# Kernel tuning notes

Hardware: AMD Instinct MI355X
Metric: run time of the kernel (lower is better)

## Reference

```python
import jax, jax.numpy as jnp
import numpy as np
from math import factorial, sqrt, pi

LMAX, NSH = 2, 9
F = 64
N_RBF = 20
N_INTER = 2
N_ATOMS = 1000
N_PAIRS = 10000
CUTOFF = 5.0

# ---------- Clebsch-Gordan coefficients for real spherical harmonics ----------

def _cg_complex(l1, m1, l2, m2, l3, m3):
    # <l1 m1 l2 m2 | l3 m3> via Racah formula
    if m3 != m1 + m2 or not (abs(l1 - l2) <= l3 <= l1 + l2):
        return 0.0
    f = factorial
    pre = sqrt((2 * l3 + 1) * f(l3 + l1 - l2) * f(l3 - l1 + l2) * f(l1 + l2 - l3) / f(l1 + l2 + l3 + 1))
    pre *= sqrt(f(l3 + m3) * f(l3 - m3) * f(l1 - m1) * f(l1 + m1) * f(l2 - m2) * f(l2 + m2))
    s = 0.0
    for k in range(l1 + l2 - l3 + 1):
        d = [k, l1 + l2 - l3 - k, l1 - m1 - k, l2 + m2 - k, l3 - l2 + m1 + k, l3 - l1 - m2 + k]
        if min(d) < 0:
            continue
        s += (-1) ** k / np.prod([float(f(t)) for t in d])
    return pre * s

def _sh_indices(lmax):
    l = np.concatenate([np.full(2 * ll + 1, ll) for ll in range(lmax + 1)])
    m = np.concatenate([np.arange(-ll, ll + 1) for ll in range(lmax + 1)])
    return l, m

def _real_cg(lmax):
    lidx, midx = _sh_indices(lmax)
    n = (lmax + 1) ** 2
    cgc = np.zeros((n, n, n))
    for a in range(n):
        for b in range(n):
            for c in range(n):
                cgc[a, b, c] = _cg_complex(lidx[a], midx[a], lidx[b], midx[b], lidx[c], midx[c])
    # complex -> real spherical harmonic change of basis (per degree l)
    U = np.zeros((n, n), dtype=np.complex128)
    for ll in range(lmax + 1):
        base = ll * ll + ll
        U[base, base] = 1.0
        for m in range(1, ll + 1):
            U[base + m, base - m] = 1 / sqrt(2)
            U[base + m, base + m] = (-1) ** m / sqrt(2)
            U[base - m, base - m] = 1j / sqrt(2)
            U[base - m, base + m] = -1j * (-1) ** m / sqrt(2)
    cgr = np.einsum('ijk,ai,bj,ck->abc', cgc.astype(np.complex128), U, U, U.conj())
    parity = (-1.0) ** lidx
    mask = (parity[:, None, None] * parity[None, :, None]) == parity[None, None, :]
    cgr = np.real(cgr) * mask
    cgr = np.transpose(cgr, (2, 0, 1))  # [s_out, s_in(x), s_filter(Y)]
    s1, s2, s3 = np.nonzero(np.abs(cgr) > 1e-9)
    return s1, s2, s3, cgr[s1, s2, s3].astype(np.float32), lidx

_S1, _S2, _S3, _CGV, _LIDX = _real_cg(LMAX)
IDX1 = jnp.asarray(_S1)            # output sh channel per CG path
IDX2 = jnp.asarray(_S2)            # input-feature sh channel per CG path
IDX3 = jnp.asarray(_S3)            # Ylm sh channel per CG path
CGVAL = jnp.asarray(_CGV)          # CG value per path
WIDX = jnp.asarray(_LIDX[_S3])     # radial-filter degree per CG path
LIDX = jnp.asarray(_LIDX)          # degree of each of the 9 sh channels

# ---------- real spherical harmonics (lmax=2, orthonormal, m=-l..l order) ----------

def _rsh(u):
    x, y, z = u[:, 0], u[:, 1], u[:, 2]
    c1 = sqrt(3.0 / (4.0 * pi))
    c2 = 0.5 * sqrt(15.0 / pi)
    return jnp.stack([
        jnp.full_like(x, 0.5 / sqrt(pi)),
        c1 * y, c1 * z, c1 * x,
        c2 * x * y,
        c2 * y * z,
        0.25 * sqrt(5.0 / pi) * (3.0 * z * z - 1.0),
        c2 * x * z,
        0.25 * sqrt(15.0 / pi) * (x * x - y * y),
    ], axis=1)


def setup_inputs() -> dict:
    key = jax.random.key(0)
    ks = jax.random.split(key, 10)
    atomic_numbers = jax.random.randint(ks[0], (N_ATOMS,), 0, 100)
    r_ij = 1.5 * jax.random.normal(ks[1], (N_PAIRS, 3), dtype=jnp.float32)
    idx_i = jnp.sort(jax.random.randint(ks[2], (N_PAIRS,), 0, N_ATOMS))
    idx_j = jax.random.randint(ks[3], (N_PAIRS,), 0, N_ATOMS)
    emb = jax.random.normal(ks[4], (100, F), dtype=jnp.float32)
    def s(k, sh, fan):
        return jax.random.normal(k, sh, dtype=jnp.float32) / float(np.sqrt(fan))
    Wf = s(ks[5], (N_INTER, N_RBF, (LMAX + 1) * F), N_RBF)
    bf = jnp.zeros((N_INTER, (LMAX + 1) * F), jnp.float32)
    W1 = s(ks[6], (N_INTER, F, F), F)
    W2 = s(ks[7], (N_INTER, F, F), F)
    W3 = s(ks[8], (N_INTER, F, F), F)
    Wg = s(ks[9], (N_INTER, F, (LMAX + 1) * F), F)
    bg = jnp.zeros((N_INTER, (LMAX + 1) * F), jnp.float32)
    return dict(atomic_numbers=atomic_numbers, r_ij=r_ij, idx_i=idx_i, idx_j=idx_j,
                emb=emb, Wf=Wf, bf=bf, W1=W1, W2=W2, W3=W3, Wg=Wg, bg=bg)


def reference(atomic_numbers, r_ij, idx_i, idx_j, emb, Wf, bf, W1, W2, W3, Wg, bg):
    n_atoms = atomic_numbers.shape[0]
    d = jnp.linalg.norm(r_ij, axis=1, keepdims=True)          # [P,1]
    Yij = _rsh(r_ij / d)                                       # [P,9]
    offsets = jnp.linspace(0.0, CUTOFF, N_RBF)                 # GaussianRBF
    width = CUTOFF / (N_RBF - 1)
    radial = jnp.exp((-0.5 / (width * width)) * (d - offsets) ** 2)   # [P,n_rbf]
    cut = 0.5 * (jnp.cos(d * (pi / CUTOFF)) + 1.0) * (d < CUTOFF)     # [P,1]
    # nuclear embedding + scalar2rsh (zero-pad l>0 channels)
    x = jnp.zeros((n_atoms, NSH, F), emb.dtype).at[:, 0, :].set(emb[atomic_numbers])
    for t in range(N_INTER):
        # SO3Convolution
        Wij = (radial @ Wf[t] + bf[t]).reshape(-1, LMAX + 1, F) * cut[:, :, None]  # [P,lmax+1,F]
        xj = x[idx_j]                                                              # [P,9,F]
        v = xj[:, IDX2] * Yij[:, IDX3, None] * Wij[:, WIDX] * CGVAL[None, :, None]  # [P,nnz,F]
        yij = jnp.zeros_like(xj).at[:, IDX1].add(v)                                 # CG scatter
        dx = jax.ops.segment_sum(yij, idx_i, num_segments=n_atoms)                  # edge->node scatter
        # mixing1 + SO3TensorProduct
        ddx = dx @ W1[t]
        tp = jnp.zeros_like(dx).at[:, IDX1].add(dx[:, IDX2] * ddx[:, IDX3] * CGVAL[None, :, None])
        dx = (dx + tp) @ W2[t]
        # SO3ParametricGatedNonlinearity (gate from l=0 channel)
        gate = (dx[:, 0] @ Wg[t] + bg[t]).reshape(-1, LMAX + 1, F)
        dx = dx * jax.nn.sigmoid(gate[:, LIDX])
        dx = dx @ W3[t]
        x = x + dx
    return x  # multipole_representation [n_atoms, 9, F]; x[:,0] is scalar_representation
```

## Files before the change

### kernel.cpp

```cpp
#include <hip/hip_runtime.h>
#include <cmath>

constexpr int kNsh    = 9;
constexpr int kF      = 64;
constexpr int kNrbf   = 20;
constexpr int kNAtoms = 1000;
constexpr int kNPairs = 10000;
constexpr float kCutoffF = 5.0f;
constexpr int kMaxNZ  = 200;
constexpr int kCp     = 12;
constexpr int kXs     = kF * kCp;
constexpr int kWT     = 68;

struct CGSparse {
  int n;
  int c[kMaxNZ];
  int a[kMaxNZ];
  int b[kMaxNZ];
  float v[kMaxNZ];
};

constexpr double cfact(int n) {
  double r = 1.0;
  for (int i = 2; i <= n; i++) r *= (double)i;
  return r;
}
constexpr double cabs_(double x) { return x < 0 ? -x : x; }
constexpr double csqrt_(double x) {
  if (x <= 0.0) return 0.0;
  double g = x < 1.0 ? 1.0 : x;
  for (int i = 0; i < 60; i++) g = 0.5 * (g + x / g);
  return g;
}

constexpr double cg_cplx(int l1, int m1, int l2, int m2, int l3, int m3) {
  if (m3 != m1 + m2) return 0.0;
  int lo = l1 > l2 ? l1 - l2 : l2 - l1;
  if (l3 < lo || l3 > l1 + l2) return 0.0;
  double pre = csqrt_((2 * l3 + 1) * cfact(l3 + l1 - l2) * cfact(l3 - l1 + l2) *
                      cfact(l1 + l2 - l3) / cfact(l1 + l2 + l3 + 1));
  pre *= csqrt_(cfact(l3 + m3) * cfact(l3 - m3) * cfact(l1 - m1) *
                cfact(l1 + m1) * cfact(l2 - m2) * cfact(l2 + m2));
  double s = 0.0;
  for (int k = 0; k <= l1 + l2 - l3; k++) {
    int d0 = k, d1 = l1 + l2 - l3 - k, d2 = l1 - m1 - k;
    int d3 = l2 + m2 - k, d4 = l3 - l2 + m1 + k, d5 = l3 - l1 - m2 + k;
    if (d0 < 0 || d1 < 0 || d2 < 0 || d3 < 0 || d4 < 0 || d5 < 0) continue;
    double den = cfact(d0) * cfact(d1) * cfact(d2) * cfact(d3) * cfact(d4) * cfact(d5);
    s += ((k % 2) ? -1.0 : 1.0) / den;
  }
  return pre * s;
}

constexpr CGSparse build_cg() {
  CGSparse out{};
  int lidx[9] = {0, 1, 1, 1, 2, 2, 2, 2, 2};
  int midx[9] = {0, -1, 0, 1, -2, -1, 0, 1, 2};
  double Ur[9][9] = {};
  double Ui[9][9] = {};
  for (int l = 0; l <= 2; l++) {
    int base = l * l + l;
    Ur[base][base] = 1.0;
    for (int m = 1; m <= l; m++) {
      double s2 = 1.0 / csqrt_(2.0);
      double sgn = (m % 2) ? -1.0 : 1.0;
      Ur[base + m][base - m] = s2;
      Ur[base + m][base + m] = sgn * s2;
      Ui[base - m][base - m] = s2;
      Ui[base - m][base + m] = -sgn * s2;
    }
  }
  double cgr[9][9][9] = {};
  for (int i = 0; i < 9; i++)
    for (int j = 0; j < 9; j++)
      for (int k = 0; k < 9; k++) {
        double cv = cg_cplx(lidx[i], midx[i], lidx[j], midx[j], lidx[k], midx[k]);
        if (cv == 0.0) continue;
        for (int a2 = 0; a2 < 9; a2++) {
          if (Ur[a2][i] == 0.0 && Ui[a2][i] == 0.0) continue;
          for (int b2 = 0; b2 < 9; b2++) {
            if (Ur[b2][j] == 0.0 && Ui[b2][j] == 0.0) continue;
            for (int c2 = 0; c2 < 9; c2++) {
              if (Ur[c2][k] == 0.0 && Ui[c2][k] == 0.0) continue;
              double ar = Ur[a2][i], ai = Ui[a2][i];
              double br = Ur[b2][j], bi = Ui[b2][j];
              double cr = Ur[c2][k], ci = -Ui[c2][k];
              double pr = ar * br - ai * bi;
              double pi = ar * bi + ai * br;
              double rr = pr * cr - pi * ci;
              cgr[c2][a2][b2] += rr * cv;
            }
          }
        }
      }
  int n = 0;
  for (int c2 = 0; c2 < 9; c2++)
    for (int a2 = 0; a2 < 9; a2++)
      for (int b2 = 0; b2 < 9; b2++) {
        bool mask = ((lidx[a2] + lidx[b2]) % 2) == (lidx[c2] % 2);
        double v = mask ? cgr[c2][a2][b2] : 0.0;
        if (cabs_(v) > 1e-9) {
          out.c[n] = c2;
          out.a[n] = a2;
          out.b[n] = b2;
          out.v[n] = (float)v;
          n++;
        }
      }
  out.n = n;
  return out;
}

constexpr CGSparse CG = build_cg();
static_assert(CG.n > 0 && CG.n <= kMaxNZ, "CG table size out of range");

constexpr int kPreBlkPairs = kNPairs / 8;
constexpr int kPreBlkSeg   = (kNAtoms + 1 + 255) / 256;
constexpr int kPreBlkTotal = kPreBlkPairs + kPreBlkSeg;

__global__ __launch_bounds__(256) void k_pre(
    const float* __restrict__ rij, const int* __restrict__ idx_i,
    float* __restrict__ pd_all, int* __restrict__ seg) {
  const int blk = blockIdx.x;
  if (blk < kPreBlkPairs) {
    int sub = threadIdx.x >> 5;
    int f = threadIdx.x & 31;
    int p = blk * 8 + sub;
    float rx = rij[3 * p + 0], ry = rij[3 * p + 1], rz = rij[3 * p + 2];
    float d = sqrtf(rx * rx + ry * ry + rz * rz);
    float inv = 1.0f / d;
    float x = rx * inv, y = ry * inv, z = rz * inv;
    const float c0 = 0.28209479177387814f;
    const float c1 = 0.4886025119029199f;
    const float c2 = 1.0925484305920792f;
    const float c3 = 0.31539156525252005f;
    const float c4 = 0.5462742152960396f;
    float cut = (d < kCutoffF) ? 0.5f * (cosf(d * (float)(M_PI / 5.0)) + 1.0f) : 0.0f;
    float val = 0.f;
    if (f < 9) {
      val =
          (f == 0) ? c0 :
          (f == 1) ? c1 * y :
          (f == 2) ? c1 * z :
          (f == 3) ? c1 * x :
          (f == 4) ? c2 * x * y :
          (f == 5) ? c2 * y * z :
          (f == 6) ? c3 * (3.0f * z * z - 1.0f) :
          (f == 7) ? c2 * x * z :
                     c4 * (x * x - y * y);
    } else if (f == 9) {
      val = cut;
    } else if (f < 30) {
      const float width = kCutoffF / (kNrbf - 1);
      const float coef = -0.5f / (width * width);
      float off = (kCutoffF * (f - 10)) / (kNrbf - 1);
      float tt = d - off;
      val = expf(coef * tt * tt) * cut;
    }
    if (f < 30) pd_all[p * 32 + f] = val;
  } else {
    int a = (blk - kPreBlkPairs) * 256 + threadIdx.x;
    if (a <= kNAtoms) {
      int lo = 0, hi = kNPairs;
      while (lo < hi) {
        int mid = (lo + hi) >> 1;
        if (idx_i[mid] < a) lo = mid + 1; else hi = mid;
      }
      seg[a] = lo;
    }
  }
}

__device__ __forceinline__ void mm_phase(const float* __restrict__ sIn,
                                         const float* __restrict__ W,
                                         float* __restrict__ sRw,
                                         int k0, int cgi, int fb) {
  if (cgi >= 3) return;
  const int c0 = cgi * 4;
  float acc[4][4];
  #pragma unroll
  for (int i = 0; i < 4; i++)
    #pragma unroll
    for (int j = 0; j < 4; j++) acc[i][j] = 0.f;
  #pragma unroll
  for (int half = 0; half < 2; half++) {
    float4 wr[8];
    #pragma unroll
    for (int kk = 0; kk < 8; kk++) {
      wr[kk] = *(const float4*)(W + (k0 + half * 8 + kk) * kF + fb);
    }
    #pragma unroll
    for (int kk = 0; kk < 8; kk++) {
      int k = k0 + half * 8 + kk;
      float4 av = *(const float4*)(sIn + k * kCp + c0);
      float4 wv = wr[kk];
      float a[4] = {av.x, av.y, av.z, av.w};
      float w[4] = {wv.x, wv.y, wv.z, wv.w};
      #pragma unroll
      for (int i = 0; i < 4; i++)
        #pragma unroll
        for (int j = 0; j < 4; j++) acc[i][j] += a[i] * w[j];
    }
  }
  #pragma unroll
  for (int j = 0; j < 4; j++) {
    float4 v = {acc[0][j], acc[1][j], acc[2][j], acc[3][j]};
    *(float4*)(sRw + (fb + j) * kCp + c0) = v;
  }
}

template <int T>
__global__ __launch_bounds__(256) void k_inter(
    const float* __restrict__ pd_all, const float* __restrict__ Wft,
    const float* __restrict__ bft, const int* __restrict__ seg,
    const int* __restrict__ idx_j, const int* __restrict__ Z,
    const float* __restrict__ emb, const float* __restrict__ x_in,
    const float* __restrict__ W1, const float* __restrict__ W2,
    const float* __restrict__ W3, const float* __restrict__ Wg,
    const float* __restrict__ bg, float* __restrict__ x_out) {
  const int atom = blockIdx.x;
  const int tid = threadIdx.x;
  const int wv = tid >> 6;
  const int lane = tid & 63;
  const int cgi = lane >> 4;
  const int fb = (lane & 15) * 4;
  const int k0 = wv * 16;

  __shared__ __align__(16) float sWfT[kF * kWT];
  __shared__ __align__(16) float sA[kF * kCp];
  __shared__ __align__(16) float sR[4][kF * kCp];
  __shared__ __align__(16) float sGp[4][192];

  {
    const float4* g4 = (const float4*)Wft;
    #pragma unroll
    for (int rr = 0; rr < 4; rr++) {
      int i = rr * 256 + tid;
      if (i < kNrbf * 192 / 4) {
        float4 v = g4[i];
        int m = 4 * i;
        int k = m / 192, rem = m % 192;
        int l = rem / 64, f0 = rem % 64;
        int li = l * 20 + k;
        float va[4] = {v.x, v.y, v.z, v.w};
        #pragma unroll
        for (int q = 0; q < 4; q++) sWfT[(f0 + q) * kWT + li] = va[q];
      }
    }
  }
  const float bf0 = bft[lane], bf1 = bft[64 + lane], bf2 = bft[128 + lane];
  __syncthreads();

  {
    float y[12];
    #pragma unroll
    for (int c = 0; c < 12; c++) y[c] = 0.f;
    const int s0 = seg[atom], s1 = seg[atom + 1];
    const float* wrow = sWfT + lane * kWT;
    for (int p0 = s0 + wv; p0 < s1; p0 += 4) {
      const int p = __builtin_amdgcn_readfirstlane(p0);
      const int j = __builtin_amdgcn_readfirstlane(idx_j[p]);
      const float* pd = pd_all + p * 32;
      const float cut = pd[9];
      float Wl[3] = {bf0 * cut, bf1 * cut, bf2 * cut};
      #pragma unroll
      for (int j4 = 0; j4 < 15; j4++) {
        float4 w = *(const float4*)(wrow + 4 * j4);
        float wa[4] = {w.x, w.y, w.z, w.w};
        #pragma unroll
        for (int q = 0; q < 4; q++) {
          constexpr int dummy = 0; (void)dummy;
          int i = 4 * j4 + q;
          Wl[i / 20] += pd[10 + (i % 20)] * wa[q];
        }
      }
      float YW[9];
      YW[0] = pd[0] * Wl[0];
      YW[1] = pd[1] * Wl[1];
      YW[2] = pd[2] * Wl[1];
      YW[3] = pd[3] * Wl[1];
      #pragma unroll
      for (int b = 4; b < 9; b++) YW[b] = pd[b] * Wl[2];
      if (T == 0) {
        float e = emb[Z[j] * kF + lane];
        #pragma unroll
        for (int q = 0; q < CG.n; q++) {
          if (CG.a[q] == 0) y[CG.c[q]] += CG.v[q] * YW[CG.b[q]] * e;
        }
      } else {
        const float* xj = x_in + j * kXs + lane * kCp;
        float xv[12];
        *(float4*)&xv[0] = *(const float4*)(xj + 0);
        *(float4*)&xv[4] = *(const float4*)(xj + 4);
        *(float4*)&xv[8] = *(const float4*)(xj + 8);
        #pragma unroll
        for (int q = 0; q < CG.n; q++) {
          y[CG.c[q]] += CG.v[q] * YW[CG.b[q]] * xv[CG.a[q]];
        }
      }
    }
    float4* r4 = (float4*)(sR[wv] + lane * kCp);
    r4[0] = *(float4*)&y[0];
    r4[1] = *(float4*)&y[4];
    r4[2] = *(float4*)&y[8];
  }
  __syncthreads();
  if (tid < 192) {
    const float4* r0 = (const float4*)sR[0];
    const float4* r1 = (const float4*)sR[1];
    const float4* r2 = (const float4*)sR[2];
    const float4* r3 = (const float4*)sR[3];
    float4 a = r0[tid], b = r1[tid], c = r2[tid], d = r3[tid];
    float4 s = {a.x + b.x + c.x + d.x, a.y + b.y + c.y + d.y,
                a.z + b.z + c.z + d.z, a.w + b.w + c.w + d.w};
    ((float4*)sA)[tid] = s;
  }
  __syncthreads();

  mm_phase(sA, W1, sR[wv], k0, cgi, fb);
  __syncthreads();

  if (wv == 0) {
    float dxv[12], ddx[12];
    {
      const float4* sa = (const float4*)(sA + lane * kCp);
      *(float4*)&dxv[0] = sa[0];
      *(float4*)&dxv[4] = sa[1];
      *(float4*)&dxv[8] = sa[2];
    }
    #pragma unroll
    for (int c = 0; c < 12; c++) {
      ddx[c] = sR[0][lane * kCp + c] + sR[1][lane * kCp + c] +
               sR[2][lane * kCp + c] + sR[3][lane * kCp + c];
    }
    float t2[12];
    #pragma unroll
    for (int c = 0; c < 9; c++) t2[c] = dxv[c];
    t2[9] = 0.f; t2[10] = 0.f; t2[11] = 0.f;
    #pragma unroll
    for (int q = 0; q < CG.n; q++) {
      t2[CG.c[q]] += CG.v[q] * dxv[CG.a[q]] * ddx[CG.b[q]];
    }
    float4* sa = (float4*)(sA + lane * kCp);
    sa[0] = *(float4*)&t2[0];
    sa[1] = *(float4*)&t2[4];
    sa[2] = *(float4*)&t2[8];
  }
  __syncthreads();

  mm_phase(sA, W2, sR[wv], k0, cgi, fb);
  __syncthreads();

  {
    float g0 = 0.f, g1 = 0.f, g2 = 0.f;
    #pragma unroll 4
    for (int kk = 0; kk < 16; kk++) {
      int k = k0 + kk;
      float a = sR[0][k * kCp] + sR[1][k * kCp] + sR[2][k * kCp] + sR[3][k * kCp];
      g0 += a * Wg[k * 192 + lane];
      g1 += a * Wg[k * 192 + 64 + lane];
      g2 += a * Wg[k * 192 + 128 + lane];
    }
    sGp[wv][lane] = g0;
    sGp[wv][64 + lane] = g1;
    sGp[wv][128 + lane] = g2;
  }
  __syncthreads();

  if (wv == 0) {
    float dx2v[12];
    #pragma unroll
    for (int c = 0; c < 12; c++) {
      dx2v[c] = sR[0][lane * kCp + c] + sR[1][lane * kCp + c] +
                sR[2][lane * kCp + c] + sR[3][lane * kCp + c];
    }
    float g0 = bg[lane] + sGp[0][lane] + sGp[1][lane] + sGp[2][lane] + sGp[3][lane];
    float g1 = bg[64 + lane] + sGp[0][64 + lane] + sGp[1][64 + lane] +
               sGp[2][64 + lane] + sGp[3][64 + lane];
    float g2 = bg[128 + lane] + sGp[0][128 + lane] + sGp[1][128 + lane] +
               sGp[2][128 + lane] + sGp[3][128 + lane];
    g0 = 1.f / (1.f + expf(-g0));
    g1 = 1.f / (1.f + expf(-g1));
    g2 = 1.f / (1.f + expf(-g2));
    float dx3[12];
    dx3[0] = dx2v[0] * g0;
    dx3[1] = dx2v[1] * g1;
    dx3[2] = dx2v[2] * g1;
    dx3[3] = dx2v[3] * g1;
    #pragma unroll
    for (int c = 4; c < 9; c++) dx3[c] = dx2v[c] * g2;
    dx3[9] = 0.f; dx3[10] = 0.f; dx3[11] = 0.f;
    float4* sa = (float4*)(sA + lane * kCp);
    sa[0] = *(float4*)&dx3[0];
    sa[1] = *(float4*)&dx3[4];
    sa[2] = *(float4*)&dx3[8];
  }
  __syncthreads();

  mm_phase(sA, W3, sR[wv], k0, cgi, fb);
  __syncthreads();

  if (T == 0) {
    if (tid < 192) {
      const int f = tid / 3, r = tid % 3;
      const float4* r0 = (const float4*)sR[0];
      const float4* r1 = (const float4*)sR[1];
      const float4* r2 = (const float4*)sR[2];
      const float4* r3 = (const float4*)sR[3];
      float4 a = r0[tid], b = r1[tid], c = r2[tid], d = r3[tid];
      float4 s = {a.x + b.x + c.x + d.x, a.y + b.y + c.y + d.y,
                  a.z + b.z + c.z + d.z, a.w + b.w + c.w + d.w};
      if (r == 0) s.x += emb[Z[atom] * kF + f];
      *(float4*)(x_out + atom * kXs + tid * 4) = s;
    }
  } else {
    if (tid < 192) {
      const float4* r0 = (const float4*)sR[0];
      const float4* r1 = (const float4*)sR[1];
      const float4* r2 = (const float4*)sR[2];
      const float4* r3 = (const float4*)sR[3];
      float4 a = r0[tid], b = r1[tid], c = r2[tid], d = r3[tid];
      float4 xi = *(const float4*)(x_in + atom * kXs + tid * 4);
      float4 s = {a.x + b.x + c.x + d.x + xi.x, a.y + b.y + c.y + d.y + xi.y,
                  a.z + b.z + c.z + d.z + xi.z, a.w + b.w + c.w + d.w + xi.w};
      ((float4*)sA)[tid] = s;
    }
    __syncthreads();
    #pragma unroll
    for (int r = 0; r < 3; r++) {
      int i = r * 256 + tid;
      if (i < kNsh * kF) {
        int c = i >> 6, f = i & 63;
        x_out[atom * (kNsh * kF) + i] = sA[f * kCp + c];
      }
    }
  }
}

extern "C" void kernel_launch(void* const* d_in, const int* in_sizes, int n_in,
                              void* d_out, int out_size, void* d_ws, size_t ws_size,
                              hipStream_t stream) {
  const int* Z        = (const int*)d_in[0];
  const float* rij    = (const float*)d_in[1];
  const int* idx_i    = (const int*)d_in[2];
  const int* idx_j    = (const int*)d_in[3];
  const float* emb    = (const float*)d_in[4];
  const float* Wf     = (const float*)d_in[5];
  const float* bf     = (const float*)d_in[6];
  const float* W1     = (const float*)d_in[7];
  const float* W2     = (const float*)d_in[8];
  const float* W3     = (const float*)d_in[9];
  const float* Wg     = (const float*)d_in[10];
  const float* bg     = (const float*)d_in[11];
  float* out = (float*)d_out;

  float* x1  = (float*)d_ws;
  float* pd  = x1 + kNAtoms * kXs;
  int*   seg = (int*)(pd + kNPairs * 32);

  k_pre<<<kPreBlkTotal, 256, 0, stream>>>(rij, idx_i, pd, seg);

  k_inter<0><<<kNAtoms, 256, 0, stream>>>(
      pd, Wf, bf, seg, idx_j, Z, emb, x1,
      W1, W2, W3, Wg, bg, x1);

  k_inter<1><<<kNAtoms, 256, 0, stream>>>(
      pd, Wf + kNrbf * 192, bf + 192, seg, idx_j, Z, emb, x1,
      W1 + kF * kF, W2 + kF * kF, W3 + kF * kF,
      Wg + kF * 192, bg + 192, out);
}
```

Measured before the change: 127.6 us.

## Fuse pair preprocessing and segment search into first interaction kernel

Removes the separate k_pre launch. The first interaction kernel now finds its own atom's segment bounds by binary search and computes the spherical harmonics, cutoff and RBF features for that atom's pairs. It writes them to global memory for the second kernel to reuse, then reads them back in the interaction loop. This saves one kernel launch and its inter-kernel gap. In exchange, each block serializes preprocessing work before its interaction phase and does two redundant binary searches per block boundary.

```diff
diff --git a/kernel.cpp b/kernel.cpp
--- a/kernel.cpp
+++ b/kernel.cpp
@@ -114,59 +114,21 @@
 constexpr CGSparse CG = build_cg();
 static_assert(CG.n > 0 && CG.n <= kMaxNZ, "CG table size out of range");
 
-constexpr int kPreBlkPairs = kNPairs / 8;
-constexpr int kPreBlkSeg   = (kNAtoms + 1 + 255) / 256;
-constexpr int kPreBlkTotal = kPreBlkPairs + kPreBlkSeg;
-
-__global__ __launch_bounds__(256) void k_pre(
-    const float* __restrict__ rij, const int* __restrict__ idx_i,
-    float* __restrict__ pd_all, int* __restrict__ seg) {
-  const int blk = blockIdx.x;
-  if (blk < kPreBlkPairs) {
-    int sub = threadIdx.x >> 5;
-    int f = threadIdx.x & 31;
-    int p = blk * 8 + sub;
-    float rx = rij[3 * p + 0], ry = rij[3 * p + 1], rz = rij[3 * p + 2];
-    float d = sqrtf(rx * rx + ry * ry + rz * rz);
-    float inv = 1.0f / d;
-    float x = rx * inv, y = ry * inv, z = rz * inv;
-    const float c0 = 0.28209479177387814f;
-    const float c1 = 0.4886025119029199f;
-    const float c2 = 1.0925484305920792f;
-    const float c3 = 0.31539156525252005f;
-    const float c4 = 0.5462742152960396f;
-    float cut = (d < kCutoffF) ? 0.5f * (cosf(d * (float)(M_PI / 5.0)) + 1.0f) : 0.0f;
-    float val = 0.f;
-    if (f < 9) {
-      val =
-          (f == 0) ? c0 :
-          (f == 1) ? c1 * y :
-          (f == 2) ? c1 * z :
-          (f == 3) ? c1 * x :
-          (f == 4) ? c2 * x * y :
-          (f == 5) ? c2 * y * z :
-          (f == 6) ? c3 * (3.0f * z * z - 1.0f) :
-          (f == 7) ? c2 * x * z :
-                     c4 * (x * x - y * y);
-    } else if (f == 9) {
-      val = cut;
-    } else if (f < 30) {
-      const float width = kCutoffF / (kNrbf - 1);
-      const float coef = -0.5f / (width * width);
-      float off = (kCutoffF * (f - 10)) / (kNrbf - 1);
-      float tt = d - off;
-      val = expf(coef * tt * tt) * cut;
-    }
-    if (f < 30) pd_all[p * 32 + f] = val;
-  } else {
-    int a = (blk - kPreBlkPairs) * 256 + threadIdx.x;
-    if (a <= kNAtoms) {
-      int lo = 0, hi = kNPairs;
-      while (lo < hi) {
-        int mid = (lo + hi) >> 1;
-        if (idx_i[mid] < a) lo = mid + 1; else hi = mid;
-      }
-      seg[a] = lo;
+__device__ __forceinline__ void stage_wft(const float* __restrict__ Wft,
+                                          float* __restrict__ sWfT, int tid) {
+  const float4* g4 = (const float4*)Wft;
+  #pragma unroll
+  for (int rr = 0; rr < 4; rr++) {
+    int i = rr * 256 + tid;
+    if (i < kNrbf * 192 / 4) {
+      float4 v = g4[i];
+      int m = 4 * i;
+      int k = m / 192, rem = m % 192;
+      int l = rem / 64, f0 = rem % 64;
+      int li = l * 20 + k;
+      float va[4] = {v.x, v.y, v.z, v.w};
+      #pragma unroll
+      for (int q = 0; q < 4; q++) sWfT[(f0 + q) * kWT + li] = va[q];
     }
   }
 }
@@ -210,11 +172,13 @@
 }
 
 template <int T>
-__global__ __launch_bounds__(256) void k_inter(
-    const float* __restrict__ pd_all, const float* __restrict__ Wft,
-    const float* __restrict__ bft, const int* __restrict__ seg,
-    const int* __restrict__ idx_j, const int* __restrict__ Z,
-    const float* __restrict__ emb, const float* __restrict__ x_in,
+__device__ __forceinline__ void interaction(
+    const float* __restrict__ sWfT, float* __restrict__ sA,
+    float (*__restrict__ sR)[kF * kCp], float (*__restrict__ sGp)[192],
+    const float* __restrict__ pd_all, const float* __restrict__ bft,
+    int s0, int s1, const int* __restrict__ idx_j,
+    const int* __restrict__ Z, const float* __restrict__ emb,
+    const float* __restrict__ x_in,
     const float* __restrict__ W1, const float* __restrict__ W2,
     const float* __restrict__ W3, const float* __restrict__ Wg,
     const float* __restrict__ bg, float* __restrict__ x_out) {
@@ -226,36 +190,12 @@
   const int fb = (lane & 15) * 4;
   const int k0 = wv * 16;
 
-  __shared__ __align__(16) float sWfT[kF * kWT];
-  __shared__ __align__(16) float sA[kF * kCp];
-  __shared__ __align__(16) float sR[4][kF * kCp];
-  __shared__ __align__(16) float sGp[4][192];
-
-  {
-    const float4* g4 = (const float4*)Wft;
-    #pragma unroll
-    for (int rr = 0; rr < 4; rr++) {
-      int i = rr * 256 + tid;
-      if (i < kNrbf * 192 / 4) {
-        float4 v = g4[i];
-        int m = 4 * i;
-        int k = m / 192, rem = m % 192;
-        int l = rem / 64, f0 = rem % 64;
-        int li = l * 20 + k;
-        float va[4] = {v.x, v.y, v.z, v.w};
-        #pragma unroll
-        for (int q = 0; q < 4; q++) sWfT[(f0 + q) * kWT + li] = va[q];
-      }
-    }
-  }
   const float bf0 = bft[lane], bf1 = bft[64 + lane], bf2 = bft[128 + lane];
-  __syncthreads();
 
   {
     float y[12];
     #pragma unroll
     for (int c = 0; c < 12; c++) y[c] = 0.f;
-    const int s0 = seg[atom], s1 = seg[atom + 1];
     const float* wrow = sWfT + lane * kWT;
     for (int p0 = s0 + wv; p0 < s1; p0 += 4) {
       const int p = __builtin_amdgcn_readfirstlane(p0);
@@ -269,7 +209,6 @@
         float wa[4] = {w.x, w.y, w.z, w.w};
         #pragma unroll
         for (int q = 0; q < 4; q++) {
-          constexpr int dummy = 0; (void)dummy;
           int i = 4 * j4 + q;
           Wl[i / 20] += pd[10 + (i % 20)] * wa[q];
         }
@@ -435,6 +374,93 @@
       }
     }
   }
+}
+
+template <int T>
+__global__ __launch_bounds__(256) void k_inter(
+    const float* __restrict__ rij, const int* __restrict__ idx_i,
+    const int* __restrict__ idx_j, const int* __restrict__ Z,
+    const float* __restrict__ emb, const float* __restrict__ Wft,
+    const float* __restrict__ bft, const float* __restrict__ W1,
+    const float* __restrict__ W2, const float* __restrict__ W3,
+    const float* __restrict__ Wg, const float* __restrict__ bg,
+    const float* __restrict__ x_in, float* __restrict__ pd_all,
+    int* __restrict__ seg, float* __restrict__ x_out) {
+  const int atom = blockIdx.x;
+  const int tid = threadIdx.x;
+
+  __shared__ __align__(16) float sWfT[kF * kWT];
+  __shared__ __align__(16) float sA[kF * kCp];
+  __shared__ __align__(16) float sR[4][kF * kCp];
+  __shared__ __align__(16) float sGp[4][192];
+  __shared__ int sSeg[2];
+
+  stage_wft(Wft, sWfT, tid);
+
+  int s0, s1;
+  if (T == 0) {
+    if (tid < 2) {
+      const int a = atom + tid;
+      int lo = 0, hi = kNPairs;
+      while (lo < hi) {
+        int mid = (lo + hi) >> 1;
+        if (idx_i[mid] < a) lo = mid + 1; else hi = mid;
+      }
+      sSeg[tid] = lo;
+      seg[a] = lo;
+    }
+    __syncthreads();
+    s0 = sSeg[0];
+    s1 = sSeg[1];
+    {
+      const int sub = tid >> 5;
+      const int f = tid & 31;
+      const int npair = s1 - s0;
+      for (int pp = sub; pp < npair; pp += 8) {
+        const int p = s0 + pp;
+        float rx = rij[3 * p + 0], ry = rij[3 * p + 1], rz = rij[3 * p + 2];
+        float d = sqrtf(rx * rx + ry * ry + rz * rz);
+        float inv = 1.0f / d;
+        float x = rx * inv, y = ry * inv, z = rz * inv;
+        const float c0 = 0.28209479177387814f;
+        const float c1 = 0.4886025119029199f;
+        const float c2 = 1.0925484305920792f;
+        const float c3 = 0.31539156525252005f;
+        const float c4 = 0.5462742152960396f;
+        float cut = (d < kCutoffF) ? 0.5f * (cosf(d * (float)(M_PI / 5.0)) + 1.0f) : 0.0f;
+        float val = 0.f;
+        if (f < 9) {
+          val =
+              (f == 0) ? c0 :
+              (f == 1) ? c1 * y :
+              (f == 2) ? c1 * z :
+              (f == 3) ? c1 * x :
+              (f == 4) ? c2 * x * y :
+              (f == 5) ? c2 * y * z :
+              (f == 6) ? c3 * (3.0f * z * z - 1.0f) :
+              (f == 7) ? c2 * x * z :
+                         c4 * (x * x - y * y);
+        } else if (f == 9) {
+          val = cut;
+        } else if (f < 30) {
+          const float width = kCutoffF / (kNrbf - 1);
+          const float coef = -0.5f / (width * width);
+          float off = (kCutoffF * (f - 10)) / (kNrbf - 1);
+          float tt = d - off;
+          val = expf(coef * tt * tt) * cut;
+        }
+        if (f < 30) pd_all[p * 32 + f] = val;
+      }
+    }
+    __syncthreads();
+  } else {
+    s0 = seg[atom];
+    s1 = seg[atom + 1];
+    __syncthreads();
+  }
+
+  interaction<T>(sWfT, sA, sR, sGp, pd_all, bft, s0, s1, idx_j, Z, emb,
+                 x_in, W1, W2, W3, Wg, bg, x_out);
 }
 
 extern "C" void kernel_launch(void* const* d_in, const int* in_sizes, int n_in,
@@ -458,14 +484,14 @@
   float* pd  = x1 + kNAtoms * kXs;
   int*   seg = (int*)(pd + kNPairs * 32);
 
-  k_pre<<<kPreBlkTotal, 256, 0, stream>>>(rij, idx_i, pd, seg);
-
   k_inter<0><<<kNAtoms, 256, 0, stream>>>(
-      pd, Wf, bf, seg, idx_j, Z, emb, x1,
-      W1, W2, W3, Wg, bg, x1);
+      rij, idx_i, idx_j, Z, emb, Wf, bf,
+      W1, W2, W3, Wg, bg,
+      (const float*)nullptr, pd, seg, x1);
 
   k_inter<1><<<kNAtoms, 256, 0, stream>>>(
-      pd, Wf + kNrbf * 192, bf + 192, seg, idx_j, Z, emb, x1,
+      rij, idx_i, idx_j, Z, emb, Wf + kNrbf * 192, bf + 192,
       W1 + kF * kF, W2 + kF * kF, W3 + kF * kF,
-      Wg + kF * 192, bg + 192, out);
-}
+      Wg + kF * 192, bg + 192,
+      x1, pd, seg, out);
+}
```

Measured after the change: 126.5 us. About the same (-0.9%).
